# Kernel optimization log

Hardware: AMD Instinct MI355X
Metric: run time of the kernel (lower is better)

The kernel has to match this reference:

```python
import jax, jax.numpy as jnp
import numpy as np

BLANK = 0
NEG = -1e30  # finite -inf surrogate, safe for grads
LCAP = 512   # max decoded-hypothesis label length (static shape cap)


def _ctc_single(lp, labels, T_len, L_len):
    """CTC negative log-likelihood for one sequence.
    lp: [T, V] log-probs; labels: [L] padded int labels (blank=0 excluded).
    """
    T, V = lp.shape
    L = labels.shape[0]
    S = 2 * L + 1  # extended label seq: blank interleaved
    ext = jnp.zeros((S,), jnp.int32).at[1::2].set(labels)
    ext_m2 = jnp.concatenate([jnp.full((2,), -1, jnp.int32), ext[:-2]])
    skip = (ext != BLANK) & (ext != ext_m2)  # s-2 transition allowed
    lp_ext = lp[:, ext]  # [T, S]
    alpha0 = jnp.full((S,), NEG, lp.dtype)
    alpha0 = alpha0.at[0].set(lp_ext[0, 0]).at[1].set(lp_ext[0, 1])
    neg1 = jnp.full((1,), NEG, lp.dtype)
    neg2 = jnp.full((2,), NEG, lp.dtype)

    def step(alpha, inp):
        lp_t, t = inp
        a1 = jnp.concatenate([neg1, alpha[:-1]])
        a2 = jnp.where(skip, jnp.concatenate([neg2, alpha[:-2]]), NEG)
        new = jnp.logaddexp(jnp.logaddexp(alpha, a1), a2) + lp_t
        # freeze lattice past this sequence's true length
        return jnp.where(t < T_len, new, alpha), None

    alphaT, _ = jax.lax.scan(step, alpha0, (lp_ext[1:], jnp.arange(1, T)))
    end = jnp.logaddexp(alphaT[2 * L_len], alphaT[2 * L_len - 1])
    return -end


def _ctc_batch(acts, labels, act_lens, label_lens):
    lp = jax.nn.log_softmax(acts, axis=-1)   # [T, B, V]
    lp = jnp.transpose(lp, (1, 0, 2))        # [B, T, V]
    return jax.vmap(_ctc_single)(lp, labels, act_lens, label_lens)


def _greedy_decode(acts, act_lens):
    """Greedy CTC decode: argmax, collapse repeats, drop blanks. Static shapes."""
    T, B, V = acts.shape
    preds = jnp.argmax(acts, axis=-1).T.astype(jnp.int32)  # [B, T]
    prev = jnp.concatenate([jnp.full((B, 1), -1, jnp.int32), preds[:, :-1]], axis=1)
    tix = jnp.arange(T)[None, :]
    new_tok = (preds != BLANK) & (preds != prev) & (tix < act_lens[:, None])
    pos = jnp.cumsum(new_tok, axis=1) - 1
    keep = new_tok & (pos < LCAP)
    buf = jnp.zeros((B, LCAP + 1), jnp.int32)
    buf = buf.at[jnp.arange(B)[:, None], jnp.where(keep, pos, LCAP)].set(preds)
    dec = buf[:, :LCAP]
    dec_lens = jnp.maximum(jnp.minimum(new_tok.sum(axis=1), LCAP), 1).astype(jnp.int32)
    return dec, dec_lens


def setup_inputs() -> dict:
    key = jax.random.key(0)
    k1, k2, k3, k4 = jax.random.split(key, 4)
    T, B, V, L = 1500, 96, 128, 256
    acts = jax.random.normal(k1, (T, B, V), jnp.float32)
    labels = jax.random.randint(k2, (B, L), 1, V).astype(jnp.int32)
    act_lens = jax.random.randint(k3, (B,), 800, T + 1).astype(jnp.int32)
    label_lens = jax.random.randint(k4, (B,), 64, L + 1).astype(jnp.int32)
    return {"acts": acts, "labels": labels, "act_lens": act_lens, "label_lens": label_lens}


def reference(acts, labels, act_lens, label_lens):
    aug_loss = 1.0
    dec_labels, dec_lens = _greedy_decode(acts, act_lens)
    cost_gt = _ctc_batch(acts, labels, act_lens, label_lens)
    cost_hyp = _ctc_batch(acts, dec_labels, act_lens, dec_lens)
    return cost_gt - cost_hyp + aug_loss  # [B] per-utterance hinge costs
```

## Files before the change

### kernel.cpp

```cpp
#include <hip/hip_runtime.h>

#define TT 1500
#define BB 96
#define VV 128
#define LGT 256
#define LCAP 512
#define NEGF (-1.0e30f)
#define L2E 1.4426950408889634f
#define LN2F 0.6931471805599453f
#define NW 11

__global__ __launch_bounds__(256) void decode_kernel(
    const float* __restrict__ acts, const int* __restrict__ act_lens,
    int* __restrict__ dec, int* __restrict__ dec_lens) {
  __shared__ int preds[TT];
  __shared__ int sc[256];
  const int b = blockIdx.x;
  const int tid = threadIdx.x;
  const int Tl = act_lens[b];
  for (int t = tid; t < Tl; t += 256) {
    const float4* r4 = (const float4*)(acts + ((size_t)t * BB + b) * VV);
    float best = -3.4e38f;
    int bi = 0;
#pragma unroll
    for (int i = 0; i < VV / 4; i++) {
      float4 v = r4[i];
      if (v.x > best) { best = v.x; bi = 4 * i; }
      if (v.y > best) { best = v.y; bi = 4 * i + 1; }
      if (v.z > best) { best = v.z; bi = 4 * i + 2; }
      if (v.w > best) { best = v.w; bi = 4 * i + 3; }
    }
    preds[t] = bi;
  }
  __syncthreads();

  int pv[6];
  bool fl[6];
  int cnt = 0;
#pragma unroll
  for (int j = 0; j < 6; j++) {
    int t = tid * 6 + j;
    bool valid = t < Tl;
    int p = valid ? preds[t] : 0;
    int pr = (t == 0) ? -1 : (valid ? preds[t - 1] : -1);
    bool f = valid && (p != 0) && (p != pr);
    pv[j] = p;
    fl[j] = f;
    cnt += f;
  }
  sc[tid] = cnt;
  __syncthreads();
  for (int off = 1; off < 256; off <<= 1) {
    int v = sc[tid];
    if (tid >= off) v += sc[tid - off];
    __syncthreads();
    sc[tid] = v;
    __syncthreads();
  }
  int pos = sc[tid] - cnt;
  int total = sc[255];
  int* db = dec + (size_t)b * LCAP;
#pragma unroll
  for (int j = 0; j < 6; j++) {
    if (fl[j]) {
      if (pos < LCAP) db[pos] = pv[j];
      pos++;
    }
  }
  if (tid == 0) {
    if (total == 0) db[0] = 0;
    dec_lens[b] = max(1, min(total, LCAP));
  }
}

__device__ __forceinline__ float shr1_negf(float x) {
  int r = __builtin_amdgcn_update_dpp(__float_as_int(NEGF), __float_as_int(x),
                                      0x138, 0xf, 0xf, false);
  return __int_as_float(r);
}

__device__ __forceinline__ float log1p2f(float x) {
  float w = __builtin_fmaf(x, 0.6666666666666666f, -0.3333333333333333f);
  float p = -0.16666666666666666f;
  p = __builtin_fmaf(p, w, 0.2f);
  p = __builtin_fmaf(p, w, -0.25f);
  p = __builtin_fmaf(p, w, 0.3333333333333333f);
  p = __builtin_fmaf(p, w, -0.5f);
  p = __builtin_fmaf(p, w, 1.0f);
  return __builtin_fmaf(p * w, L2E, 0.5849625007211562f);
}

__global__ __launch_bounds__(64 * NW, 1) void ctc_kernel(
    const float* __restrict__ acts, const int* __restrict__ labels_gt,
    const int* __restrict__ act_lens, const int* __restrict__ label_lens,
    const int* __restrict__ dec, const int* __restrict__ dec_lens,
    float* __restrict__ ends) {
  __shared__ float xall[2 * LCAP + 2];
  __shared__ float fin[2];
  const int b = blockIdx.x >> 1;
  const int hyp = blockIdx.x & 1;
  const int Tl = act_lens[b];
  const int len = hyp ? dec_lens[b] : label_lens[b];
  const int* lab = hyp ? (dec + (size_t)b * LCAP) : (labels_gt + (size_t)b * LGT);
  const int S = 2 * len + 1;
  const float* act_b = acts + (size_t)b * VV;
  const int Tlm1 = Tl - 1;

  const int tid = threadIdx.x;
  const int lane = tid & 63, wv = tid >> 6;
  const int oS = 2 * ((S + 2 * NW - 1) / (2 * NW));
  const int Se = (S + 1) & ~1;
  const int o0 = min(wv * oS, Se);
  const int o1 = min(o0 + oS, S);
  const int p0 = max(0, o0 - 26);
  const int s0 = p0 + 2 * lane;
  const int s1 = s0 + 1;

  int e1 = 0;
  bool skip = false;
  if (s1 < S) {
    int li = s1 >> 1;
    e1 = lab[li];
    if (s1 >= 3) skip = (e1 != 0) && (e1 != lab[li - 1]);
  }

  float a0 = NEGF, a1 = NEGF;
  if (wv == 0 && lane == 0) {
    a0 = act_b[0] * L2E;
    a1 = act_b[e1] * L2E;
  }

  float gL0, gL1, gL2, gL3, gL4, gL5;
  float gB0, gB1, gB2, gB3, gB4, gB5;

#define PREF(GL, GB, ROW)                                  \
  {                                                        \
    const float* rp_ = act_b + (size_t)(ROW) * (BB * VV);  \
    GB = rp_[0];                                           \
    GL = rp_[e1];                                          \
  }

#define STEPK(GL, GB)                                                     \
  {                                                                       \
    float pe = shr1_negf(a1);                                             \
                              \
    float m0 = fmaxf(a0, pe);                                             \
    float d0 = fminf(a0, pe) - m0;                                        \
    float u = m0 + log1p2f(__builtin_exp2f(d0));                          \
                                  \
    float w = skip ? u : a0;                                              \
    float m1 = fmaxf(a1, w);                                              \
    float d1 = fminf(a1, w) - m1;                                         \
    float v = m1 + log1p2f(__builtin_exp2f(d1));                          \
    a0 = __builtin_fmaf(GB, L2E, u);                                      \
    a1 = __builtin_fmaf(GL, L2E, v);                                      \
  }

#define REFRESH()                                        \
  {                                                      \
    asm volatile("s_waitcnt lgkmcnt(0)" ::: "memory");   \
    __builtin_amdgcn_s_barrier();                        \
    if (s0 >= o0 && s0 < o1) xall[s0] = a0;              \
    if (s1 >= o0 && s1 < o1) xall[s1] = a1;              \
    asm volatile("s_waitcnt lgkmcnt(0)" ::: "memory");   \
    __builtin_amdgcn_s_barrier();                        \
    if (s0 < o0) {                                       \
      a0 = xall[s0];                                     \
      a1 = (s1 < S) ? xall[s1] : NEGF;                   \
    }                                                    \
  }

#define W1(OFF, GL, GB)                    \
  STEPK(GL, GB);                           \
  PREF(GL, GB, min(t + (OFF) + 6, Tlm1));

#define T1(GL, GB)                         \
  STEPK(GL, GB);                           \
  PREF(GL, GB, min(t + 6, Tlm1));          \
  ++t;                                     \
  if (t >= Tl) break;

  PREF(gL0, gB0, min(1, Tlm1));
  PREF(gL1, gB1, min(2, Tlm1));
  PREF(gL2, gB2, min(3, Tlm1));
  PREF(gL3, gB3, min(4, Tlm1));
  PREF(gL4, gB4, min(5, Tlm1));
  PREF(gL5, gB5, min(6, Tlm1));

  int t = 1;
  while (t + 12 <= Tl) {
    W1(0, gL0, gB0)
    W1(1, gL1, gB1)
    W1(2, gL2, gB2)
    W1(3, gL3, gB3)
    W1(4, gL4, gB4)
    W1(5, gL5, gB5)
    W1(6, gL0, gB0)
    W1(7, gL1, gB1)
    W1(8, gL2, gB2)
    W1(9, gL3, gB3)
    W1(10, gL4, gB4)
    W1(11, gL5, gB5)
    t += 12;
    REFRESH();
  }
  while (t < Tl) {
    T1(gL0, gB0)
    T1(gL1, gB1)
    T1(gL2, gB2)
    T1(gL3, gB3)
    T1(gL4, gB4)
    T1(gL5, gB5)
  }
#undef T1
#undef W1
#undef REFRESH
#undef STEPK
#undef PREF

  __syncthreads();
  if (s0 >= o0 && s0 < o1 && s0 == 2 * len) fin[0] = a0;
  if (s1 >= o0 && s1 < o1 && s1 == 2 * len - 1) fin[1] = a1;
  __syncthreads();
  if (tid == 0) {
    float a = fin[0], c = fin[1];
    float m = fmaxf(a, c);
    float e = m + __builtin_log2f(__builtin_exp2f(a - m) + __builtin_exp2f(c - m));
    ends[hyp * BB + b] = e;
  }
}

__global__ void final_kernel(const float* __restrict__ ends,
                             float* __restrict__ out) {
  int b = threadIdx.x;
  if (b < BB) out[b] = (ends[BB + b] - ends[b]) * LN2F + 1.0f;
}

extern "C" void kernel_launch(void* const* d_in, const int* in_sizes, int n_in,
                              void* d_out, int out_size, void* d_ws,
                              size_t ws_size, hipStream_t stream) {
  const float* acts = (const float*)d_in[0];
  const int* labels = (const int*)d_in[1];
  const int* act_lens = (const int*)d_in[2];
  const int* label_lens = (const int*)d_in[3];
  float* out = (float*)d_out;

  char* ws = (char*)d_ws;
  int* dec = (int*)ws;
  int* dec_lens = (int*)(ws + (size_t)BB * LCAP * 4);
  float* ends = (float*)(ws + (size_t)BB * LCAP * 4 + BB * 4);

  decode_kernel<<<dim3(BB), dim3(256), 0, stream>>>(acts, act_lens, dec, dec_lens);
  ctc_kernel<<<dim3(2 * BB), dim3(64 * NW), 84 * 1024, stream>>>(
      acts, labels, act_lens, label_lens, dec, dec_lens, ends);
  final_kernel<<<dim3(1), dim3(128), 0, stream>>>(ends, out);
}
```

Baseline: 356.8 us.

## Double-buffer halo exchange and widen refresh interval to sixteen steps

The halo-exchange shared buffer becomes double-buffered, which removes the first barrier in each refresh. Refreshes now happen every 16 timesteps instead of 12, with the ghost overlap widened from 26 to 34 lattice states. The prefetch depth of activation rows grows from 6 to 8. This cuts barrier count per timestep at the cost of more redundant overlap computation per wave and more registers.

```diff
diff --git a/kernel.cpp b/kernel.cpp
--- a/kernel.cpp
+++ b/kernel.cpp
@@ -9,6 +9,8 @@
 #define L2E 1.4426950408889634f
 #define LN2F 0.6931471805599453f
 #define NW 11
+#define GH 34
+#define HREF 16
 
 __global__ __launch_bounds__(256) void decode_kernel(
     const float* __restrict__ acts, const int* __restrict__ act_lens,
@@ -95,7 +97,7 @@
     const int* __restrict__ act_lens, const int* __restrict__ label_lens,
     const int* __restrict__ dec, const int* __restrict__ dec_lens,
     float* __restrict__ ends) {
-  __shared__ float xall[2 * LCAP + 2];
+  __shared__ float xall[2][2 * LCAP + 2];
   __shared__ float fin[2];
   const int b = blockIdx.x >> 1;
   const int hyp = blockIdx.x & 1;
@@ -112,7 +114,7 @@
   const int Se = (S + 1) & ~1;
   const int o0 = min(wv * oS, Se);
   const int o1 = min(o0 + oS, S);
-  const int p0 = max(0, o0 - 26);
+  const int p0 = max(0, o0 - GH);
   const int s0 = p0 + 2 * lane;
   const int s1 = s0 + 1;
 
@@ -130,8 +132,8 @@
     a1 = act_b[e1] * L2E;
   }
 
-  float gL0, gL1, gL2, gL3, gL4, gL5;
-  float gB0, gB1, gB2, gB3, gB4, gB5;
+  float gL0, gL1, gL2, gL3, gL4, gL5, gL6, gL7;
+  float gB0, gB1, gB2, gB3, gB4, gB5, gB6, gB7;
 
 #define PREF(GL, GB, ROW)                                  \
   {                                                        \
@@ -156,27 +158,26 @@
     a1 = __builtin_fmaf(GL, L2E, v);                                      \
   }
 
-#define REFRESH()                                        \
+#define REFRESH(K)                                       \
   {                                                      \
-    asm volatile("s_waitcnt lgkmcnt(0)" ::: "memory");   \
-    __builtin_amdgcn_s_barrier();                        \
-    if (s0 >= o0 && s0 < o1) xall[s0] = a0;              \
-    if (s1 >= o0 && s1 < o1) xall[s1] = a1;              \
+    float* xs = xall[(K)&1];                             \
+    if (s0 >= o0 && s0 < o1) xs[s0] = a0;                \
+    if (s1 >= o0 && s1 < o1) xs[s1] = a1;                \
     asm volatile("s_waitcnt lgkmcnt(0)" ::: "memory");   \
     __builtin_amdgcn_s_barrier();                        \
     if (s0 < o0) {                                       \
-      a0 = xall[s0];                                     \
-      a1 = (s1 < S) ? xall[s1] : NEGF;                   \
+      a0 = xs[s0];                                       \
+      a1 = (s1 < S) ? xs[s1] : NEGF;                     \
     }                                                    \
   }
 
 #define W1(OFF, GL, GB)                    \
   STEPK(GL, GB);                           \
-  PREF(GL, GB, min(t + (OFF) + 6, Tlm1));
+  PREF(GL, GB, min(t + (OFF) + 8, Tlm1));
 
 #define T1(GL, GB)                         \
   STEPK(GL, GB);                           \
-  PREF(GL, GB, min(t + 6, Tlm1));          \
+  PREF(GL, GB, min(t + 8, Tlm1));          \
   ++t;                                     \
   if (t >= Tl) break;
 
@@ -186,23 +187,30 @@
   PREF(gL3, gB3, min(4, Tlm1));
   PREF(gL4, gB4, min(5, Tlm1));
   PREF(gL5, gB5, min(6, Tlm1));
-
-  int t = 1;
-  while (t + 12 <= Tl) {
+  PREF(gL6, gB6, min(7, Tlm1));
+  PREF(gL7, gB7, min(8, Tlm1));
+
+  int t = 1, k = 0;
+  while (t + HREF <= Tl) {
     W1(0, gL0, gB0)
     W1(1, gL1, gB1)
     W1(2, gL2, gB2)
     W1(3, gL3, gB3)
     W1(4, gL4, gB4)
     W1(5, gL5, gB5)
-    W1(6, gL0, gB0)
-    W1(7, gL1, gB1)
-    W1(8, gL2, gB2)
-    W1(9, gL3, gB3)
-    W1(10, gL4, gB4)
-    W1(11, gL5, gB5)
-    t += 12;
-    REFRESH();
+    W1(6, gL6, gB6)
+    W1(7, gL7, gB7)
+    W1(8, gL0, gB0)
+    W1(9, gL1, gB1)
+    W1(10, gL2, gB2)
+    W1(11, gL3, gB3)
+    W1(12, gL4, gB4)
+    W1(13, gL5, gB5)
+    W1(14, gL6, gB6)
+    W1(15, gL7, gB7)
+    t += HREF;
+    ++k;
+    REFRESH(k);
   }
   while (t < Tl) {
     T1(gL0, gB0)
@@ -211,6 +219,8 @@
     T1(gL3, gB3)
     T1(gL4, gB4)
     T1(gL5, gB5)
+    T1(gL6, gB6)
+    T1(gL7, gB7)
   }
 #undef T1
 #undef W1
@@ -251,7 +261,7 @@
   float* ends = (float*)(ws + (size_t)BB * LCAP * 4 + BB * 4);
 
   decode_kernel<<<dim3(BB), dim3(256), 0, stream>>>(acts, act_lens, dec, dec_lens);
-  ctc_kernel<<<dim3(2 * BB), dim3(64 * NW), 84 * 1024, stream>>>(
+  ctc_kernel<<<dim3(2 * BB), dim3(64 * NW), 80 * 1024, stream>>>(
       acts, labels, act_lens, label_lens, dec, dec_lens, ends);
   final_kernel<<<dim3(1), dim3(128), 0, stream>>>(ends, out);
 }
```

Measured after the change: 347.9 us (median of 2 runs). 2.5% less time.
